# Kernel tuning notes

Measured on AMD Instinct MI355X. Metric: run time of the kernel, lower is better.

Reference implementation:

```python
import jax, jax.numpy as jnp
import numpy as np

N, C, H, W = 2, 32, 56, 56   # batch, in_channels, spatial
O = 64                        # out_channels
PAD = 1                       # ConstantPad2d padding


def _shift(a, dh, dw):
    """Zero-padded shift: out[..., i, j] = a[..., i+dh, j+dw] (out of range -> 0)."""
    nd = a.ndim
    if dh:
        a = jnp.pad(a[..., dh:, :], [(0, 0)] * (nd - 2) + [(0, dh), (0, 0)])
    if dw:
        a = jnp.pad(a[..., :, dw:], [(0, 0)] * (nd - 2) + [(0, 0), (0, dw)])
    return a


def setup_inputs() -> dict:
    key = jax.random.key(0)
    k1, k2, k3 = jax.random.split(key, 3)
    x = jax.random.normal(k1, (N, C, H, W), dtype=jnp.float32)
    # weight entries are used as divisors in extract_param_p; keep them bounded
    # away from zero (magnitude in [0.5, 1.5], random sign) for a stable baseline.
    mag = jax.random.uniform(k2, (O, C, 3, 3), minval=0.5, maxval=1.5, dtype=jnp.float32)
    sgn = jnp.where(jax.random.bernoulli(k3, 0.5, (O, C, 3, 3)), 1.0, -1.0).astype(jnp.float32)
    return {"x": x, "weight": mag * sgn}


def reference(x, weight):
    w = weight  # [O, C, 3, 3]
    # --- extract predict filter P = [p0, p1, p2, p3], each [O, C] ---
    p0 = -w[:, :, 2, 0] / w[:, :, 2, 1]
    p1 = -w[:, :, 0, 2] / w[:, :, 1, 2]
    p2 = (1.0 - w[:, :, 0, 0]
          + w[:, :, 2, 0] * w[:, :, 0, 1] / w[:, :, 2, 1]
          + w[:, :, 0, 2] * w[:, :, 1, 0] / w[:, :, 1, 2]) / w[:, :, 1, 1]
    p3 = -w[:, :, 2, 2] / w[:, :, 1, 1]
    # --- extract update filter U = [u0..u4], each [O, C] ---
    u0, u1, u2, u3, u4 = (w[:, :, 0, 1], w[:, :, 2, 1],
                          w[:, :, 1, 0], w[:, :, 1, 2], w[:, :, 1, 1])

    def bc(c):  # [O, C] -> broadcastable over [N, O, C, Hp, Wp]
        return c[None, :, :, None, None]

    # forward: ConstantPad2d then vanilla lifting scheme (aux_index = 2).
    xp = jnp.pad(x, ((0, 0), (0, 0), (PAD, PAD), (PAD, PAD)))  # [N, C, Hp, Wp]
    x5 = xp[:, None, :, :, :]                                  # [N, 1, C, Hp, Wp]

    x0 = x5
    x1 = _shift(x5, 0, 1)
    x2 = _shift(x5, 1, 0)
    x3 = _shift(x5, 1, 1)
    x0_2 = _shift(x5, 2, 2)

    # predict steps (broadcast to [N, O, C, Hp, Wp])
    x1 = x1 - bc(p0) * x0
    x2 = x2 - bc(p1) * x0
    x3 = x3 - bc(p2) * x0 - bc(p3) * x0_2

    x1_2 = _shift(x1, 2, 0)
    x2_2 = _shift(x2, 0, 2)

    # update steps
    out = (x0
           + bc(u0) * x1 + bc(u1) * x1_2
           + bc(u2) * x2 + bc(u3) * x2_2
           + bc(u4) * x3)

    # crop aux_index=2 border, then sum over in_channels (channel_split loop
    # processes contiguous O slices and concatenates -> identical to full O).
    return out[:, :, :, :-2, :-2].sum(axis=2)  # [N, O, H, W]
```

## Files before the change

### kernel.cpp

```cpp
#include <hip/hip_runtime.h>


namespace {
constexpr int Cc = 32, Hh = 56, Ww = 56, Oo = 64;

constexpr int RSTRIDE = 10;
constexpr int REGION  = 576;

__global__ __launch_bounds__(1024, 4)
void lifting_conv_kernel(const float* __restrict__ x,
                         const float* __restrict__ w,
                         float* __restrict__ out)
{
    __shared__ float xs[Cc * 4 * 60];

    const int tid  = threadIdx.x;
    const int og   = blockIdx.x;
    const int ip   = blockIdx.y;
    const int n    = blockIdx.z;
    const int i0   = ip * 2;
    const int lane = tid & 63;
    const int wv   = tid >> 6;

    {
        const int col = lane - 1;
        const bool cok = (lane < 58) && ((unsigned)col < (unsigned)Ww);
        float v[8];
        #pragma unroll
        for (int p = 0; p < 8; ++p) {
            const int rowid = p * 16 + wv;
            const int r = rowid & 3;
            const int h = i0 - 1 + r;
            v[p] = 0.0f;
            if (cok && (unsigned)h < (unsigned)Hh)
                v[p] = x[((n * Cc + (rowid >> 2)) * Hh + h) * Ww + col];
        }
        if (lane < 58) {
            #pragma unroll
            for (int p = 0; p < 8; ++p)
                xs[(p * 16 + wv) * 60 + lane] = v[p];
        }
    }
    __syncthreads();

    const int oq   = wv & 3;
    const int cch  = wv >> 2;
    const bool act = lane < 56;
    const int lact = act ? lane : 0;
    const int rsub = (lact >= 28) ? 1 : 0;
    const int cp   = lact - rsub * 28;
    const int col0 = cp * 2;

    const int o_base = __builtin_amdgcn_readfirstlane(og * 16 + oq * 4);
    const int cbeg   = __builtin_amdgcn_readfirstlane(cch * 8);
    const float* __restrict__ wb = w + ((size_t)o_base * Cc + cbeg) * 9;

    float acc[4][2];
    #pragma unroll
    for (int i = 0; i < 4; ++i) { acc[i][0] = 0.f; acc[i][1] = 0.f; }

    const float* xbase = &xs[cbeg * 240 + rsub * 60 + col0];

    float2 a0 = *(const float2*)(xbase);
    float2 a1 = *(const float2*)(xbase + 2);
    float2 b0 = *(const float2*)(xbase + 60);
    float2 b1 = *(const float2*)(xbase + 62);
    float2 d0 = *(const float2*)(xbase + 120);
    float2 d1 = *(const float2*)(xbase + 122);

    #pragma unroll 2
    for (int cc = 0; cc < 8; ++cc) {
        const float2 r0a = a0, r0b = a1,
                     r1a = b0, r1b = b1,
                     r2a = d0, r2b = d1;
        if (cc < 7) {
            const float* xn = xbase + (cc + 1) * 240;
            a0 = *(const float2*)(xn);
            a1 = *(const float2*)(xn + 2);
            b0 = *(const float2*)(xn + 60);
            b1 = *(const float2*)(xn + 62);
            d0 = *(const float2*)(xn + 120);
            d1 = *(const float2*)(xn + 122);
        }
        #pragma unroll
        for (int oo = 0; oo < 4; ++oo) {
            const float* wc = wb + (oo * Cc + cc) * 9;
            const float w0 = wc[0], w1 = wc[1], w2 = wc[2],
                        w3 = wc[3], w4 = wc[4], w5 = wc[5],
                        w6 = wc[6], w7 = wc[7], w8 = wc[8];
            acc[oo][0] += w0 * r0a.x + w1 * r0a.y + w2 * r0b.x
                        + w3 * r1a.x + w4 * r1a.y + w5 * r1b.x
                        + w6 * r2a.x + w7 * r2a.y + w8 * r2b.x;
            acc[oo][1] += w0 * r0a.y + w1 * r0b.x + w2 * r0b.y
                        + w3 * r1a.y + w4 * r1b.x + w5 * r1b.y
                        + w6 * r2a.y + w7 * r2b.x + w8 * r2b.y;
        }
    }

    __syncthreads();

    if (cch > 0 && act) {
        float* p = &xs[((cch - 1) * 4 + oq) * REGION + lane * RSTRIDE];
        #pragma unroll
        for (int oo = 0; oo < 4; ++oo)
            *(float2*)(p + oo * 2) = make_float2(acc[oo][0], acc[oo][1]);
    }
    __syncthreads();

    if (cch == 0 && act) {
        #pragma unroll
        for (int pi = 0; pi < 3; ++pi) {
            const float* p = &xs[(pi * 4 + oq) * REGION + lane * RSTRIDE];
            #pragma unroll
            for (int oo = 0; oo < 4; ++oo) {
                const float2 v = *(const float2*)(p + oo * 2);
                acc[oo][0] += v.x;
                acc[oo][1] += v.y;
            }
        }
        const int row = i0 + rsub;
        #pragma unroll
        for (int oo = 0; oo < 4; ++oo) {
            float2 v; v.x = acc[oo][0]; v.y = acc[oo][1];
            *(float2*)(out + ((size_t)(n * Oo + o_base + oo) * Hh + row) * Ww + col0) = v;
        }
    }
}
}

extern "C" void kernel_launch(void* const* d_in, const int* in_sizes, int n_in,
                              void* d_out, int out_size, void* d_ws, size_t ws_size,
                              hipStream_t stream)
{
    const float* x = (const float*)d_in[0];
    const float* w = (const float*)d_in[1];
    float* out = (float*)d_out;

    dim3 grid(4, 28, 2);
    lifting_conv_kernel<<<grid, 1024, 0, stream>>>(x, w, out);
}
```

Measured before the change: 62.95 us.

## Halve block size, double grid, use separate reduction buffer and drop prefetch

Blocks shrink from 1024 to 512 threads, each covering 8 output channels instead of 16, and the grid doubles to 448 blocks so more blocks can spread across CUs. The cross-wave partial-sum reduction now goes to a dedicated shared buffer, which removes one __syncthreads barrier. The software prefetch of the next channel's input is replaced by plain per-iteration loads. In exchange, each block reloads the full input tile into LDS, so total staging work doubles, and per-block LDS use grows.

New measurement: 64.61 us. +2.6%, slower.

```diff
diff --git a/kernel.cpp b/kernel.cpp
--- a/kernel.cpp
+++ b/kernel.cpp
@@ -5,14 +5,15 @@
 constexpr int Cc = 32, Hh = 56, Ww = 56, Oo = 64;
 
 constexpr int RSTRIDE = 10;
-constexpr int REGION  = 576;
+constexpr int REGION  = 560;
 
-__global__ __launch_bounds__(1024, 4)
+__global__ __launch_bounds__(512, 4)
 void lifting_conv_kernel(const float* __restrict__ x,
                          const float* __restrict__ w,
                          float* __restrict__ out)
 {
     __shared__ float xs[Cc * 4 * 60];
+    __shared__ float rs[6 * REGION];
 
     const int tid  = threadIdx.x;
     const int og   = blockIdx.x;
@@ -25,10 +26,10 @@
     {
         const int col = lane - 1;
         const bool cok = (lane < 58) && ((unsigned)col < (unsigned)Ww);
-        float v[8];
+        float v[16];
         #pragma unroll
-        for (int p = 0; p < 8; ++p) {
-            const int rowid = p * 16 + wv;
+        for (int p = 0; p < 16; ++p) {
+            const int rowid = p * 8 + wv;
             const int r = rowid & 3;
             const int h = i0 - 1 + r;
             v[p] = 0.0f;
@@ -37,21 +38,21 @@
         }
         if (lane < 58) {
             #pragma unroll
-            for (int p = 0; p < 8; ++p)
-                xs[(p * 16 + wv) * 60 + lane] = v[p];
+            for (int p = 0; p < 16; ++p)
+                xs[(p * 8 + wv) * 60 + lane] = v[p];
         }
     }
     __syncthreads();
 
-    const int oq   = wv & 3;
-    const int cch  = wv >> 2;
+    const int oq   = wv & 1;
+    const int cch  = wv >> 1;
     const bool act = lane < 56;
     const int lact = act ? lane : 0;
     const int rsub = (lact >= 28) ? 1 : 0;
     const int cp   = lact - rsub * 28;
     const int col0 = cp * 2;
 
-    const int o_base = __builtin_amdgcn_readfirstlane(og * 16 + oq * 4);
+    const int o_base = __builtin_amdgcn_readfirstlane(og * 8 + oq * 4);
     const int cbeg   = __builtin_amdgcn_readfirstlane(cch * 8);
     const float* __restrict__ wb = w + ((size_t)o_base * Cc + cbeg) * 9;
 
@@ -61,27 +62,16 @@
 
     const float* xbase = &xs[cbeg * 240 + rsub * 60 + col0];
 
-    float2 a0 = *(const float2*)(xbase);
-    float2 a1 = *(const float2*)(xbase + 2);
-    float2 b0 = *(const float2*)(xbase + 60);
-    float2 b1 = *(const float2*)(xbase + 62);
-    float2 d0 = *(const float2*)(xbase + 120);
-    float2 d1 = *(const float2*)(xbase + 122);
-
     #pragma unroll 2
     for (int cc = 0; cc < 8; ++cc) {
-        const float2 r0a = a0, r0b = a1,
-                     r1a = b0, r1b = b1,
-                     r2a = d0, r2b = d1;
-        if (cc < 7) {
-            const float* xn = xbase + (cc + 1) * 240;
-            a0 = *(const float2*)(xn);
-            a1 = *(const float2*)(xn + 2);
-            b0 = *(const float2*)(xn + 60);
-            b1 = *(const float2*)(xn + 62);
-            d0 = *(const float2*)(xn + 120);
-            d1 = *(const float2*)(xn + 122);
-        }
+        const float* xr = xbase + cc * 240;
+        const float2 r0a = *(const float2*)(xr);
+        const float2 r0b = *(const float2*)(xr + 2);
+        const float2 r1a = *(const float2*)(xr + 60);
+        const float2 r1b = *(const float2*)(xr + 62);
+        const float2 r2a = *(const float2*)(xr + 120);
+        const float2 r2b = *(const float2*)(xr + 122);
+
         #pragma unroll
         for (int oo = 0; oo < 4; ++oo) {
             const float* wc = wb + (oo * Cc + cc) * 9;
@@ -97,10 +87,8 @@
         }
     }
 
-    __syncthreads();
-
     if (cch > 0 && act) {
-        float* p = &xs[((cch - 1) * 4 + oq) * REGION + lane * RSTRIDE];
+        float* p = &rs[((cch - 1) * 2 + oq) * REGION + lane * RSTRIDE];
         #pragma unroll
         for (int oo = 0; oo < 4; ++oo)
             *(float2*)(p + oo * 2) = make_float2(acc[oo][0], acc[oo][1]);
@@ -110,7 +98,7 @@
     if (cch == 0 && act) {
         #pragma unroll
         for (int pi = 0; pi < 3; ++pi) {
-            const float* p = &xs[(pi * 4 + oq) * REGION + lane * RSTRIDE];
+            const float* p = &rs[(pi * 2 + oq) * REGION + lane * RSTRIDE];
             #pragma unroll
             for (int oo = 0; oo < 4; ++oo) {
                 const float2 v = *(const float2*)(p + oo * 2);
@@ -136,6 +124,6 @@
     const float* w = (const float*)d_in[1];
     float* out = (float*)d_out;
 
-    dim3 grid(4, 28, 2);
-    lifting_conv_kernel<<<grid, 1024, 0, stream>>>(x, w, out);
+    dim3 grid(8, 28, 2);
+    lifting_conv_kernel<<<grid, 512, 0, stream>>>(x, w, out);
 }
```
